# Kernel tuning notes

Hardware: AMD Instinct MI355X
Metric: run time of the kernel (lower is better)

The kernel has to match this reference:

```python
import jax, jax.numpy as jnp
import numpy as np

N, E, B, S = 8192, 65536, 8, 64
V, R, D = 100000, 38, 768  # concept vocab, relations (self-loop id = R), sent_dim


def setup_inputs() -> dict:
    key = jax.random.key(0)
    ks = jax.random.split(key, 10)
    concept_ids = jax.random.randint(ks[0], (N,), 0, V)
    edge_index = jax.random.randint(ks[1], (2, E), 0, N)
    rel = jax.random.randint(ks[2], (E,), 0, R).astype(jnp.float32)
    wgt = jax.random.uniform(ks[3], (E,), dtype=jnp.float32)
    edge_attr = jnp.stack([rel, wgt], axis=1)  # [E, 2]: (relation_id, weight)
    # sentence concept ids drawn from the actual subgraph so the mask is non-trivial
    pos = jax.random.randint(ks[4], (B, S), 0, N)
    sent_concept_ids = concept_ids[pos]
    concept_embedding = jax.random.normal(ks[5], (V, D), dtype=jnp.float32) * 0.02
    relation_embedding = jax.random.normal(ks[6], (R, D), dtype=jnp.float32) * 0.02
    self_loop_embedding = jax.random.normal(ks[7], (D,), dtype=jnp.float32) * 0.02
    W = jax.random.normal(ks[8], (3 * D, D), dtype=jnp.float32) * 0.02  # lin weight (in, out)
    b = jnp.zeros((D,), dtype=jnp.float32)
    return dict(concept_ids=concept_ids, edge_index=edge_index, edge_attr=edge_attr,
                sent_concept_ids=sent_concept_ids, concept_embedding=concept_embedding,
                relation_embedding=relation_embedding, self_loop_embedding=self_loop_embedding,
                W=W, b=b)


def reference(concept_ids, edge_index, edge_attr, sent_concept_ids,
              concept_embedding, relation_embedding, self_loop_embedding, W, b):
    n = concept_ids.shape[0]
    d = concept_embedding.shape[1]
    self_loop_id = relation_embedding.shape[0]

    # node features: concept embedding gather (settings.no_gnn=True path)
    x = concept_embedding[concept_ids]                     # [N, d]

    edge_rel = edge_attr[:, 0].astype(jnp.int32)           # [E]
    edge_w = edge_attr[:, 1]                               # [E]
    ea = edge_w[:, None] * relation_embedding[edge_rel]    # [E, d]

    # append self-loops
    loop = jnp.arange(n, dtype=edge_index.dtype)
    ei = jnp.concatenate([edge_index, jnp.stack([loop, loop])], axis=1)   # [2, E+N]
    ea = jnp.concatenate([ea, jnp.broadcast_to(self_loop_embedding, (n, d))], axis=0)
    rel_full = jnp.concatenate([edge_rel, jnp.full((n,), self_loop_id, dtype=jnp.int32)])

    head, tail = ei[0], ei[1]
    # singles_to_triples: [x_head | edge_attr | x_tail]
    triples = jnp.concatenate([x[head], ea, x[tail]], axis=1)             # [T, 3d]
    encoded_triples = triples @ W + b                                     # [T, d]

    head_ids = concept_ids[head]
    tail_ids = concept_ids[tail]
    triple_ids = jnp.stack([head_ids, rel_full.astype(concept_ids.dtype), tail_ids], axis=1)

    # membership mask: sentence i covers triple t if head or tail concept in its id set
    hm = (sent_concept_ids[:, :, None] == head_ids[None, None, :]).any(axis=1)  # [B, T]
    tm = (sent_concept_ids[:, :, None] == tail_ids[None, None, :]).any(axis=1)
    mask = hm | tm
    return encoded_triples, mask, triple_ids
```

## Files before the change

kernel.cpp:

```cpp
#include <hip/hip_runtime.h>
#include <stdint.h>

#define N_NODES 8192
#define N_EDGES 65536
#define N_TRIPLES (N_EDGES + N_NODES)
#define D 768
#define D2 1536
#define NREL 38
#define BATCH 8
#define SENTN 512
#define OUT1_OFF ((size_t)N_TRIPLES * D)
#define OUT2_OFF (OUT1_OFF + (size_t)BATCH * N_TRIPLES)

typedef __attribute__((ext_vector_type(4))) float f32x4;
typedef __attribute__((ext_vector_type(2))) float f32x2;
typedef __attribute__((ext_vector_type(4))) unsigned short ushort4v;

static __device__ __forceinline__ unsigned short f2bf(float f) {
  unsigned u = __builtin_bit_cast(unsigned, f);
  u += 0x7FFFu + ((u >> 16) & 1u);
  return (unsigned short)(u >> 16);
}

__global__ void k_prep(const int* __restrict__ cids, const float* __restrict__ cemb,
                       unsigned char* __restrict__ x8,
                       const float* __restrict__ W, unsigned char* __restrict__ wt8,
                       const float* __restrict__ relemb, const float* __restrict__ selfemb,
                       float* __restrict__ partials,
                       const int* __restrict__ sent, unsigned int* __restrict__ nmask) {
  __shared__ __align__(16) char smraw[32 * 33 * 4];
  int b = blockIdx.x;
  if (b < 6144) {
    int t4 = b * 256 + threadIdx.x;
    int row = t4 / (D / 4);
    int c4 = t4 % (D / 4);
    int cid = cids[row];
    float4 v = ((const float4*)(cemb + (size_t)cid * D))[c4];
    int p = __builtin_amdgcn_cvt_pk_fp8_f32(v.x, v.y, 0, false);
    p = __builtin_amdgcn_cvt_pk_fp8_f32(v.z, v.w, p, true);
    *(int*)(x8 + (size_t)t4 * 4) = p;
  } else if (b < 7296) {
    float (*tile)[33] = (float(*)[33])smraw;
    int idx = b - 6144;
    int kb = (idx % 24) * 32;
    int jb = (idx / 24) * 32;
    int tx = threadIdx.x % 32;
    int ty = threadIdx.x / 32;
#pragma unroll
    for (int i = 0; i < 4; ++i) {
      int k = kb + ty + i * 8;
      int j = jb + tx;
      float v = (j < D) ? W[(size_t)k * D + j] : W[(size_t)(2 * D + k) * D + (j - D)];
      tile[ty + i * 8][tx] = v;
    }
    __syncthreads();
#pragma unroll
    for (int i = 0; i < 4; ++i) {
      int j = jb + ty + i * 8;
      int k = kb + tx;
      float v = tile[tx][ty + i * 8];
      wt8[(size_t)j * D + k] =
          (unsigned char)(__builtin_amdgcn_cvt_pk_fp8_f32(v, v, 0, false) & 0xFF);
    }
  } else if (b < 7530) {
    int idx = b - 7296;
    int r = idx / 6;
    int ch = idx % 6;
    const float* src = (r < NREL) ? (relemb + (size_t)r * D) : selfemb;
    int c = threadIdx.x;
    const float* W2 = W + (size_t)D * D;
    float a0 = 0.f, a1 = 0.f, a2 = 0.f;
    int k0 = ch * 128;
    for (int k = 0; k < 128; ++k) {
      float s = src[k0 + k];
      const float* wr = W2 + (size_t)(k0 + k) * D;
      a0 += s * wr[c];
      a1 += s * wr[c + 256];
      a2 += s * wr[c + 512];
    }
    float* p = partials + (size_t)idx * D;
    p[c] = a0;
    p[c + 256] = a1;
    p[c + 512] = a2;
  } else {
    int* ls = (int*)smraw;
    for (int i = threadIdx.x; i < SENTN; i += 256) ls[i] = sent[i];
    __syncthreads();
    int n = (b - 7530) * 256 + threadIdx.x;
    int cid = cids[n];
    unsigned m = 0;
#pragma unroll 16
    for (int s = 0; s < SENTN; ++s)
      m |= (ls[s] == cid) ? (1u << (s >> 6)) : 0u;
    nmask[n] = m;
  }
}

__global__ void k_gemm(const unsigned char* __restrict__ A,
                       const unsigned char* __restrict__ BT,
                       unsigned char* __restrict__ xw8,
                       const float* __restrict__ partials, float* __restrict__ relw2,
                       const float* __restrict__ bias,
                       const int* __restrict__ cids, const int* __restrict__ eidx,
                       const float* __restrict__ eattr, const unsigned* __restrict__ nmask,
                       float* __restrict__ out) {
  __shared__ __align__(16) unsigned char lsAB[2][2][128 * 64];
  const int bid = blockIdx.x;
  const int tid = threadIdx.x;

  if (bid >= 768) {
    if (bid < 807) {
      int r = bid - 768;
      int c = tid;
      const float* p = partials + (size_t)r * 6 * D;
#pragma unroll
      for (int j = 0; j < 3; ++j) {
        int cc = c + j * 256;
        float s = 0.f;
#pragma unroll
        for (int ch = 0; ch < 6; ++ch) s += p[(size_t)ch * D + cc];
        relw2[(size_t)r * D + cc] = s;
      }
    } else {
      int t = (bid - 807) * 256 + tid;
      int h, tl;
      float rel;
      if (t < N_EDGES) {
        h = eidx[t];
        tl = eidx[N_EDGES + t];
        rel = (float)(int)eattr[2 * t];
      } else {
        h = t - N_EDGES;
        tl = h;
        rel = (float)NREL;
      }
      float* o2 = out + OUT2_OFF + (size_t)t * 3;
      __builtin_nontemporal_store((float)cids[h], o2 + 0);
      __builtin_nontemporal_store(rel, o2 + 1);
      __builtin_nontemporal_store((float)cids[tl], o2 + 2);
      unsigned m = nmask[h] | nmask[tl];
      float* o1 = out + OUT1_OFF;
#pragma unroll
      for (int bb = 0; bb < BATCH; ++bb)
        __builtin_nontemporal_store(((m >> bb) & 1u) ? 1.0f : 0.0f,
                                    o1 + (size_t)bb * N_TRIPLES + t);
    }
    return;
  }

  const int lane = tid & 63;
  const int wid = tid >> 6;
  const int wr = wid >> 1, wc = wid & 1;

  const int swz = (bid & 7) * 96 + (bid >> 3);
  const int arow0 = (swz / 12) * 128;
  const int bcol0 = (swz % 12) * 128;

  f32x4 acc[4][4] = {};

  const int rloc = tid >> 2;
  const int gpair = (tid & 3) ^ ((rloc >> 1) & 3);
  const unsigned char* ga = A + (size_t)(arow0 + rloc) * D + gpair * 16;
  const unsigned char* gb = BT + (size_t)(bcol0 + rloc) * D + gpair * 16;

  const int lr = lane & 15;
  const int hi = lane >> 4;
  const int fsw = (lr >> 1) & 3;

#define STAGE(BUF, K0)                                                                 \
  {                                                                                    \
    _Pragma("unroll") for (int c = 0; c < 2; ++c) {                                    \
      __builtin_amdgcn_global_load_lds(                                                \
          (const __attribute__((address_space(1))) void*)(ga + (size_t)c * 64 * D + (K0)), \
          (__attribute__((address_space(3))) void*)(&lsAB[BUF][0][c * 4096 + tid * 16]), \
          16, 0, 0);                                                                   \
      __builtin_amdgcn_global_load_lds(                                                \
          (const __attribute__((address_space(1))) void*)(gb + (size_t)c * 64 * D + (K0)), \
          (__attribute__((address_space(3))) void*)(&lsAB[BUF][1][c * 4096 + tid * 16]), \
          16, 0, 0);                                                                   \
    }                                                                                  \
  }

#define COMPUTE(BUF)                                                                   \
  {                                                                                    \
    const unsigned char* sA = lsAB[BUF][0];                                            \
    const unsigned char* sB = lsAB[BUF][1];                                            \
    _Pragma("unroll") for (int kk = 0; kk < 2; ++kk) {                                 \
      const int pair = kk * 2 + (hi >> 1);                                             \
      const int boff = ((pair ^ fsw) * 16) + (hi & 1) * 8;                             \
      long af[4], bfv[4];                                                              \
      _Pragma("unroll") for (int m = 0; m < 4; ++m)                                    \
          af[m] = *(const long*)(sA + (wr * 64 + m * 16 + lr) * 64 + boff);            \
      _Pragma("unroll") for (int n = 0; n < 4; ++n)                                    \
          bfv[n] = *(const long*)(sB + (wc * 64 + n * 16 + lr) * 64 + boff);           \
      _Pragma("unroll") for (int m = 0; m < 4; ++m)                                    \
          _Pragma("unroll") for (int n = 0; n < 4; ++n)                                \
              acc[m][n] = __builtin_amdgcn_mfma_f32_16x16x32_fp8_fp8(af[m], bfv[n],    \
                                                                     acc[m][n], 0, 0, 0); \
    }                                                                                  \
  }

  STAGE(0, 0)
  STAGE(1, 64)
#pragma unroll
  for (int t = 0; t < 12; ++t) {
    if (t < 11) { asm volatile("s_waitcnt vmcnt(4)" ::: "memory"); }
    else        { asm volatile("s_waitcnt vmcnt(0)" ::: "memory"); }
    __builtin_amdgcn_s_barrier();
    if (t & 1) COMPUTE(1) else COMPUTE(0)
    asm volatile("" ::: "memory");
    __builtin_amdgcn_s_barrier();
    if (t + 2 < 12) { if (t & 1) STAGE(1, (t + 2) * 64) else STAGE(0, (t + 2) * 64) }
  }
#undef STAGE
#undef COMPUTE

  const int crow = hi * 4;
  const int ccol = lr;
  const bool addb = (bcol0 < D);
#pragma unroll
  for (int m = 0; m < 4; ++m) {
    int row = arow0 + wr * 64 + m * 16 + crow;
#pragma unroll
    for (int n = 0; n < 4; ++n) {
      int col = bcol0 + wc * 64 + n * 16 + ccol;
      float bv = addb ? bias[col] : 0.f;
      unsigned char* cp = xw8 + (size_t)row * D2 + col;
      int p01 = __builtin_amdgcn_cvt_pk_fp8_f32(acc[m][n][0] + bv, acc[m][n][1] + bv, 0, false);
      int p23 = __builtin_amdgcn_cvt_pk_fp8_f32(acc[m][n][2] + bv, acc[m][n][3] + bv, 0, false);
      cp[0] = (unsigned char)(p01 & 0xFF);
      cp[(size_t)1 * D2] = (unsigned char)((p01 >> 8) & 0xFF);
      cp[(size_t)2 * D2] = (unsigned char)(p23 & 0xFF);
      cp[(size_t)3 * D2] = (unsigned char)((p23 >> 8) & 0xFF);
    }
  }
}

__global__ void k_out(const int* __restrict__ eidx, const float* __restrict__ eattr,
                      const unsigned char* __restrict__ xw8, const float* __restrict__ relw2,
                      float* __restrict__ out) {
  const int wid = threadIdx.x >> 6;
  const int lane = threadIdx.x & 63;
  const int t0 = blockIdx.x * 16 + wid * 4;

  const unsigned* r1[4];
  const unsigned* r3[4];
  const f32x4* rw[4];
  float w[4];
#pragma unroll
  for (int q = 0; q < 4; ++q) {
    int t = t0 + q;
    if (t < N_EDGES) {
      int h = eidx[t];
      int tl = eidx[N_EDGES + t];
      int rel = (int)eattr[2 * t];
      w[q] = eattr[2 * t + 1];
      r1[q] = (const unsigned*)(xw8 + (size_t)h * D2);
      r3[q] = (const unsigned*)(xw8 + (size_t)tl * D2 + D);
      rw[q] = (const f32x4*)(relw2 + (size_t)rel * D);
    } else {
      int i = t - N_EDGES;
      w[q] = 1.f;
      r1[q] = (const unsigned*)(xw8 + (size_t)i * D2);
      r3[q] = (const unsigned*)(xw8 + (size_t)i * D2 + D);
      rw[q] = (const f32x4*)(relw2 + (size_t)NREL * D);
    }
  }

#pragma unroll
  for (int j = 0; j < 3; ++j) {
    const int c4 = j * 64 + lane;
    unsigned ua[4], ux[4];
    f32x4 c[4];
#pragma unroll
    for (int q = 0; q < 4; ++q) {
      ua[q] = r1[q][c4];
      ux[q] = r3[q][c4];
      c[q] = rw[q][c4];
    }
#pragma unroll
    for (int q = 0; q < 4; ++q) {
      f32x2 alo = __builtin_amdgcn_cvt_pk_f32_fp8(ua[q], false);
      f32x2 ahi = __builtin_amdgcn_cvt_pk_f32_fp8(ua[q], true);
      f32x2 xlo = __builtin_amdgcn_cvt_pk_f32_fp8(ux[q], false);
      f32x2 xhi = __builtin_amdgcn_cvt_pk_f32_fp8(ux[q], true);
      f32x4 res;
      res.x = alo[0] + w[q] * c[q].x + xlo[0];
      res.y = alo[1] + w[q] * c[q].y + xlo[1];
      res.z = ahi[0] + w[q] * c[q].z + xhi[0];
      res.w = ahi[1] + w[q] * c[q].w + xhi[1];
      f32x4* o = (f32x4*)(out + (size_t)(t0 + q) * D);
      __builtin_nontemporal_store(res, &o[c4]);
    }
  }
}

extern "C" void kernel_launch(void* const* d_in, const int* in_sizes, int n_in,
                              void* d_out, int out_size, void* d_ws, size_t ws_size,
                              hipStream_t stream) {
  const int* cids = (const int*)d_in[0];
  const int* eidx = (const int*)d_in[1];
  const float* eattr = (const float*)d_in[2];
  const int* sent = (const int*)d_in[3];
  const float* cemb = (const float*)d_in[4];
  const float* relemb = (const float*)d_in[5];
  const float* selfemb = (const float*)d_in[6];
  const float* W = (const float*)d_in[7];
  const float* bias = (const float*)d_in[8];

  char* ws = (char*)d_ws;
  unsigned char* x8 = (unsigned char*)ws;
  unsigned char* wt8 = (unsigned char*)(ws + 6291456);
  unsigned char* xw8 = (unsigned char*)(ws + 6291456 + 1179648);
  float* relw2 = (float*)(ws + 20054016);
  unsigned* nmask = (unsigned*)(ws + 20054016 + 119808);
  float* partials = (float*)(ws + 20054016 + 119808 + 32768);

  float* out = (float*)d_out;

  k_prep<<<dim3(7562), dim3(256), 0, stream>>>(cids, cemb, x8, W, wt8, relemb, selfemb,
                                               partials, sent, nmask);
  k_gemm<<<dim3(1095), dim3(256), 0, stream>>>(x8, wt8, xw8, partials, relw2, bias,
                                               cids, eidx, eattr, nmask, out);
  k_out<<<dim3(N_TRIPLES / 16), dim3(256), 0, stream>>>(eidx, eattr, xw8, relw2, out);
}
```

Measured before the change: 96.69 us.

## Enlarge GEMM tile to 256x128 with 512 threads and grid-stride prep kernel

The FP8 GEMM block tile grows from 128x128 to 256x128 with 8 waves per block, so each staged B tile is reused across twice as many A rows and the grid shrinks to 384 GEMM blocks plus the auxiliary blocks. The wait count drops to match three loads per stage. The prep kernel becomes a grid-stride loop over 2048 persistent blocks instead of 7562 one-shot blocks. The aim is to cut global and LDS traffic per FLOP and launch overhead, at the cost of more LDS per block, lower occupancy, and fewer blocks to fill the CUs.

```diff
diff --git a/kernel.cpp b/kernel.cpp
--- a/kernel.cpp
+++ b/kernel.cpp
@@ -29,70 +29,72 @@
                        float* __restrict__ partials,
                        const int* __restrict__ sent, unsigned int* __restrict__ nmask) {
   __shared__ __align__(16) char smraw[32 * 33 * 4];
-  int b = blockIdx.x;
-  if (b < 6144) {
-    int t4 = b * 256 + threadIdx.x;
-    int row = t4 / (D / 4);
-    int c4 = t4 % (D / 4);
-    int cid = cids[row];
-    float4 v = ((const float4*)(cemb + (size_t)cid * D))[c4];
-    int p = __builtin_amdgcn_cvt_pk_fp8_f32(v.x, v.y, 0, false);
-    p = __builtin_amdgcn_cvt_pk_fp8_f32(v.z, v.w, p, true);
-    *(int*)(x8 + (size_t)t4 * 4) = p;
-  } else if (b < 7296) {
-    float (*tile)[33] = (float(*)[33])smraw;
-    int idx = b - 6144;
-    int kb = (idx % 24) * 32;
-    int jb = (idx / 24) * 32;
-    int tx = threadIdx.x % 32;
-    int ty = threadIdx.x / 32;
-#pragma unroll
-    for (int i = 0; i < 4; ++i) {
-      int k = kb + ty + i * 8;
-      int j = jb + tx;
-      float v = (j < D) ? W[(size_t)k * D + j] : W[(size_t)(2 * D + k) * D + (j - D)];
-      tile[ty + i * 8][tx] = v;
-    }
+  for (int b = blockIdx.x; b < 7562; b += 2048) {
     __syncthreads();
-#pragma unroll
-    for (int i = 0; i < 4; ++i) {
-      int j = jb + ty + i * 8;
-      int k = kb + tx;
-      float v = tile[tx][ty + i * 8];
-      wt8[(size_t)j * D + k] =
-          (unsigned char)(__builtin_amdgcn_cvt_pk_fp8_f32(v, v, 0, false) & 0xFF);
-    }
-  } else if (b < 7530) {
-    int idx = b - 7296;
-    int r = idx / 6;
-    int ch = idx % 6;
-    const float* src = (r < NREL) ? (relemb + (size_t)r * D) : selfemb;
-    int c = threadIdx.x;
-    const float* W2 = W + (size_t)D * D;
-    float a0 = 0.f, a1 = 0.f, a2 = 0.f;
-    int k0 = ch * 128;
-    for (int k = 0; k < 128; ++k) {
-      float s = src[k0 + k];
-      const float* wr = W2 + (size_t)(k0 + k) * D;
-      a0 += s * wr[c];
-      a1 += s * wr[c + 256];
-      a2 += s * wr[c + 512];
-    }
-    float* p = partials + (size_t)idx * D;
-    p[c] = a0;
-    p[c + 256] = a1;
-    p[c + 512] = a2;
-  } else {
-    int* ls = (int*)smraw;
-    for (int i = threadIdx.x; i < SENTN; i += 256) ls[i] = sent[i];
-    __syncthreads();
-    int n = (b - 7530) * 256 + threadIdx.x;
-    int cid = cids[n];
-    unsigned m = 0;
+    if (b < 6144) {
+      int t4 = b * 256 + threadIdx.x;
+      int row = t4 / (D / 4);
+      int c4 = t4 % (D / 4);
+      int cid = cids[row];
+      float4 v = ((const float4*)(cemb + (size_t)cid * D))[c4];
+      int p = __builtin_amdgcn_cvt_pk_fp8_f32(v.x, v.y, 0, false);
+      p = __builtin_amdgcn_cvt_pk_fp8_f32(v.z, v.w, p, true);
+      *(int*)(x8 + (size_t)t4 * 4) = p;
+    } else if (b < 7296) {
+      float (*tile)[33] = (float(*)[33])smraw;
+      int idx = b - 6144;
+      int kb = (idx % 24) * 32;
+      int jb = (idx / 24) * 32;
+      int tx = threadIdx.x % 32;
+      int ty = threadIdx.x / 32;
+#pragma unroll
+      for (int i = 0; i < 4; ++i) {
+        int k = kb + ty + i * 8;
+        int j = jb + tx;
+        float v = (j < D) ? W[(size_t)k * D + j] : W[(size_t)(2 * D + k) * D + (j - D)];
+        tile[ty + i * 8][tx] = v;
+      }
+      __syncthreads();
+#pragma unroll
+      for (int i = 0; i < 4; ++i) {
+        int j = jb + ty + i * 8;
+        int k = kb + tx;
+        float v = tile[tx][ty + i * 8];
+        wt8[(size_t)j * D + k] =
+            (unsigned char)(__builtin_amdgcn_cvt_pk_fp8_f32(v, v, 0, false) & 0xFF);
+      }
+    } else if (b < 7530) {
+      int idx = b - 7296;
+      int r = idx / 6;
+      int ch = idx % 6;
+      const float* src = (r < NREL) ? (relemb + (size_t)r * D) : selfemb;
+      int c = threadIdx.x;
+      const float* W2 = W + (size_t)D * D;
+      float a0 = 0.f, a1 = 0.f, a2 = 0.f;
+      int k0 = ch * 128;
+      for (int k = 0; k < 128; ++k) {
+        float s = src[k0 + k];
+        const float* wr = W2 + (size_t)(k0 + k) * D;
+        a0 += s * wr[c];
+        a1 += s * wr[c + 256];
+        a2 += s * wr[c + 512];
+      }
+      float* p = partials + (size_t)idx * D;
+      p[c] = a0;
+      p[c + 256] = a1;
+      p[c + 512] = a2;
+    } else {
+      int* ls = (int*)smraw;
+      for (int i = threadIdx.x; i < SENTN; i += 256) ls[i] = sent[i];
+      __syncthreads();
+      int n = (b - 7530) * 256 + threadIdx.x;
+      int cid = cids[n];
+      unsigned m = 0;
 #pragma unroll 16
-    for (int s = 0; s < SENTN; ++s)
-      m |= (ls[s] == cid) ? (1u << (s >> 6)) : 0u;
-    nmask[n] = m;
+      for (int s = 0; s < SENTN; ++s)
+        m |= (ls[s] == cid) ? (1u << (s >> 6)) : 0u;
+      nmask[n] = m;
+    }
   }
 }
 
@@ -104,25 +106,27 @@
                        const int* __restrict__ cids, const int* __restrict__ eidx,
                        const float* __restrict__ eattr, const unsigned* __restrict__ nmask,
                        float* __restrict__ out) {
-  __shared__ __align__(16) unsigned char lsAB[2][2][128 * 64];
+  __shared__ __align__(16) unsigned char lsA[2][256 * 64];
+  __shared__ __align__(16) unsigned char lsB[2][128 * 64];
   const int bid = blockIdx.x;
   const int tid = threadIdx.x;
 
-  if (bid >= 768) {
-    if (bid < 807) {
-      int r = bid - 768;
-      int c = tid;
+  if (bid >= 384) {
+    if (bid < 423) {
+      int r = bid - 384;
       const float* p = partials + (size_t)r * 6 * D;
 #pragma unroll
-      for (int j = 0; j < 3; ++j) {
-        int cc = c + j * 256;
-        float s = 0.f;
-#pragma unroll
-        for (int ch = 0; ch < 6; ++ch) s += p[(size_t)ch * D + cc];
-        relw2[(size_t)r * D + cc] = s;
+      for (int j = 0; j < 2; ++j) {
+        int cc = tid + j * 512;
+        if (cc < D) {
+          float s = 0.f;
+#pragma unroll
+          for (int ch = 0; ch < 6; ++ch) s += p[(size_t)ch * D + cc];
+          relw2[(size_t)r * D + cc] = s;
+        }
       }
     } else {
-      int t = (bid - 807) * 256 + tid;
+      int t = (bid - 423) * 512 + tid;
       int h, tl;
       float rel;
       if (t < N_EDGES) {
@@ -150,18 +154,18 @@
 
   const int lane = tid & 63;
   const int wid = tid >> 6;
-  const int wr = wid >> 1, wc = wid & 1;
-
-  const int swz = (bid & 7) * 96 + (bid >> 3);
-  const int arow0 = (swz / 12) * 128;
+  const int wr = wid >> 1;
+  const int wc = wid & 1;
+
+  const int swz = (bid & 7) * 48 + (bid >> 3);
+  const int arow0 = (swz / 12) * 256;
   const int bcol0 = (swz % 12) * 128;
 
   f32x4 acc[4][4] = {};
 
-  const int rloc = tid >> 2;
-  const int gpair = (tid & 3) ^ ((rloc >> 1) & 3);
-  const unsigned char* ga = A + (size_t)(arow0 + rloc) * D + gpair * 16;
-  const unsigned char* gb = BT + (size_t)(bcol0 + rloc) * D + gpair * 16;
+  const int gpair = (tid & 3) ^ ((tid >> 3) & 3);
+  const unsigned char* ga = A + (size_t)(arow0 + (tid >> 2)) * D + gpair * 16;
+  const unsigned char* gb = BT + (size_t)(bcol0 + (tid >> 2)) * D + gpair * 16;
 
   const int lr = lane & 15;
   const int hi = lane >> 4;
@@ -169,22 +173,20 @@
 
 #define STAGE(BUF, K0)                                                                 \
   {                                                                                    \
-    _Pragma("unroll") for (int c = 0; c < 2; ++c) {                                    \
+    _Pragma("unroll") for (int c = 0; c < 2; ++c)                                      \
       __builtin_amdgcn_global_load_lds(                                                \
-          (const __attribute__((address_space(1))) void*)(ga + (size_t)c * 64 * D + (K0)), \
-          (__attribute__((address_space(3))) void*)(&lsAB[BUF][0][c * 4096 + tid * 16]), \
+          (const __attribute__((address_space(1))) void*)(ga + (size_t)c * 128 * D + (K0)), \
+          (__attribute__((address_space(3))) void*)(&lsA[BUF][c * 8192 + tid * 16]),   \
           16, 0, 0);                                                                   \
-      __builtin_amdgcn_global_load_lds(                                                \
-          (const __attribute__((address_space(1))) void*)(gb + (size_t)c * 64 * D + (K0)), \
-          (__attribute__((address_space(3))) void*)(&lsAB[BUF][1][c * 4096 + tid * 16]), \
-          16, 0, 0);                                                                   \
-    }                                                                                  \
+    __builtin_amdgcn_global_load_lds(                                                  \
+        (const __attribute__((address_space(1))) void*)(gb + (K0)),                    \
+        (__attribute__((address_space(3))) void*)(&lsB[BUF][tid * 16]), 16, 0, 0);     \
   }
 
 #define COMPUTE(BUF)                                                                   \
   {                                                                                    \
-    const unsigned char* sA = lsAB[BUF][0];                                            \
-    const unsigned char* sB = lsAB[BUF][1];                                            \
+    const unsigned char* sA = lsA[BUF];                                                \
+    const unsigned char* sB = lsB[BUF];                                                \
     _Pragma("unroll") for (int kk = 0; kk < 2; ++kk) {                                 \
       const int pair = kk * 2 + (hi >> 1);                                             \
       const int boff = ((pair ^ fsw) * 16) + (hi & 1) * 8;                             \
@@ -204,7 +206,7 @@
   STAGE(1, 64)
 #pragma unroll
   for (int t = 0; t < 12; ++t) {
-    if (t < 11) { asm volatile("s_waitcnt vmcnt(4)" ::: "memory"); }
+    if (t < 11) { asm volatile("s_waitcnt vmcnt(3)" ::: "memory"); }
     else        { asm volatile("s_waitcnt vmcnt(0)" ::: "memory"); }
     __builtin_amdgcn_s_barrier();
     if (t & 1) COMPUTE(1) else COMPUTE(0)
@@ -216,14 +218,13 @@
 #undef COMPUTE
 
   const int crow = hi * 4;
-  const int ccol = lr;
   const bool addb = (bcol0 < D);
 #pragma unroll
   for (int m = 0; m < 4; ++m) {
     int row = arow0 + wr * 64 + m * 16 + crow;
 #pragma unroll
     for (int n = 0; n < 4; ++n) {
-      int col = bcol0 + wc * 64 + n * 16 + ccol;
+      int col = bcol0 + wc * 64 + n * 16 + lr;
       float bv = addb ? bias[col] : 0.f;
       unsigned char* cp = xw8 + (size_t)row * D2 + col;
       int p01 = __builtin_amdgcn_cvt_pk_fp8_f32(acc[m][n][0] + bv, acc[m][n][1] + bv, 0, false);
@@ -318,9 +319,9 @@
 
   float* out = (float*)d_out;
 
-  k_prep<<<dim3(7562), dim3(256), 0, stream>>>(cids, cemb, x8, W, wt8, relemb, selfemb,
+  k_prep<<<dim3(2048), dim3(256), 0, stream>>>(cids, cemb, x8, W, wt8, relemb, selfemb,
                                                partials, sent, nmask);
-  k_gemm<<<dim3(1095), dim3(256), 0, stream>>>(x8, wt8, xw8, partials, relw2, bias,
-                                               cids, eidx, eattr, nmask, out);
+  k_gemm<<<dim3(567), dim3(512), 0, stream>>>(x8, wt8, xw8, partials, relw2, bias,
+                                              cids, eidx, eattr, nmask, out);
   k_out<<<dim3(N_TRIPLES / 16), dim3(256), 0, stream>>>(eidx, eattr, xw8, relw2, out);
 }
```

Result: faster. 94.26 us (-2.5%).
